# Optimization experiments

Hardware: AMD Instinct MI355X
Metric: run time of the kernel (lower is better)

The kernel has to match this reference:

```python
import jax, jax.numpy as jnp
import numpy as np

N_NODES = 50000
N_EDGES = 640000  # directed; edges (2i, 2i+1) are mutual reverses
NODE_DIM = 128
EDGE_DIM = 16
UNITS = 128
EDGE_STEPS = 4
NODE_STEPS = 4


def setup_inputs() -> dict:
    key = jax.random.key(0)
    ks = jax.random.split(key, 8)
    n_pairs = N_EDGES // 2
    a = jax.random.randint(ks[0], (n_pairs,), 0, N_NODES, dtype=jnp.int32)
    b = jax.random.randint(ks[1], (n_pairs,), 0, N_NODES, dtype=jnp.int32)
    # interleave so edge 2i = a->b and edge 2i+1 = b->a (reverse pair)
    edge_src = jnp.stack([a, b], axis=1).reshape(-1)
    edge_dst = jnp.stack([b, a], axis=1).reshape(-1)
    rev_edge = (jnp.arange(N_EDGES, dtype=jnp.int32) ^ 1)
    node_feature = jax.random.normal(ks[2], (N_NODES, NODE_DIM), jnp.float32)
    edge_feature = jax.random.normal(ks[3], (N_EDGES, EDGE_DIM), jnp.float32)
    d_in = NODE_DIM + EDGE_DIM
    W_init = jax.random.normal(ks[4], (d_in, UNITS), jnp.float32) / np.sqrt(d_in)
    b_init = jnp.zeros((UNITS,), jnp.float32)
    W_upd = jax.random.normal(ks[5], (UNITS, UNITS), jnp.float32) / np.sqrt(UNITS)
    b_upd = jnp.zeros((UNITS,), jnp.float32)
    d_node_out = UNITS + NODE_DIM
    W_node = jax.random.normal(ks[6], (d_node_out, d_node_out), jnp.float32) / np.sqrt(d_node_out)
    b_node = jnp.zeros((d_node_out,), jnp.float32)
    epsilon = jnp.zeros((), jnp.float32)
    return dict(node_feature=node_feature, edge_feature=edge_feature,
                edge_src=edge_src, edge_dst=edge_dst, rev_edge=rev_edge,
                W_init=W_init, b_init=b_init, W_upd=W_upd, b_upd=b_upd,
                W_node=W_node, b_node=b_node, epsilon=epsilon)


def reference(node_feature, edge_feature, edge_src, edge_dst, rev_edge,
              W_init, b_init, W_upd, b_upd, W_node, b_node, epsilon):
    N = node_feature.shape[0]
    # initial edge projection: concat(src node feat, edge feat) -> units, relu
    h = jax.nn.relu(
        jnp.concatenate([node_feature[edge_src], edge_feature], axis=-1) @ W_init + b_init
    )  # [E, units]
    # directed edge message passing (D-MPNN style)
    for _ in range(EDGE_STEPS):
        agg = jax.ops.segment_sum(h, edge_dst, num_segments=N)        # [N, units]
        message = agg[edge_src] - h[rev_edge]                          # exclude reverse edge
        h = jax.nn.relu(message @ W_upd + b_upd + h)
    # aggregate edges to nodes, concat with original node features
    msg = jax.ops.segment_sum(h, edge_dst, num_segments=N)             # [N, units]
    x = jnp.concatenate([node_feature, msg], axis=-1)                  # [N, units+node_dim]
    x0 = (x * (1.0 + epsilon)) @ W_node + b_node                       # GIN-style initial
    # node message passing: sum-aggregate neighbors + residual initial
    for _ in range(NODE_STEPS):
        x = jax.ops.segment_sum(x[edge_src], edge_dst, num_segments=N) + x0
    return x
```

## Files before the change

### kernel.cpp

```cpp
#include <hip/hip_runtime.h>
#include <stdint.h>

#define N_NODES 50000
#define N_EDGES 640000
#define NODE_DIM 128
#define EDGE_DIM 16
#define UNITS 128
#define DOUT 256
#define SCAN_NB ((N_NODES + 255) / 256)

typedef __attribute__((ext_vector_type(4))) float v4f;
typedef __attribute__((ext_vector_type(8))) short v8s;
typedef __attribute__((ext_vector_type(4))) short v4s;
typedef __attribute__((ext_vector_type(2))) unsigned v2u;
typedef __attribute__((ext_vector_type(4))) unsigned v4u;

static __device__ __forceinline__ short f2bf(float f) {
    return (short)((__float_as_uint(f) + 0x8000u) >> 16);
}
static __device__ __forceinline__ float bf2f(short s) {
    return __uint_as_float(((unsigned)(unsigned short)s) << 16);
}
static __device__ __forceinline__ unsigned pack_bf2(float a, float b) {
    unsigned ua = __float_as_uint(a) + 0x8000u;
    unsigned ub = __float_as_uint(b) + 0x8000u;
    return __builtin_amdgcn_perm(ub, ua, 0x07060302);
}

__global__ void k_zero(int* __restrict__ p, int n) {
    int i = blockIdx.x * 256 + threadIdx.x;
    if (i < n) p[i] = 0;
}

__global__ void k_hist(const int* __restrict__ dst, int* __restrict__ counts) {
    int e = blockIdx.x * 256 + threadIdx.x;
    if (e < N_EDGES) atomicAdd(&counts[dst[e]], 1);
}

__global__ __launch_bounds__(256) void k_scan_part(const int* __restrict__ counts,
                                                   int* __restrict__ part) {
    __shared__ int red[256];
    int t = threadIdx.x;
    int i = blockIdx.x * 256 + t;
    red[t] = (i < N_NODES) ? counts[i] : 0;
    __syncthreads();
#pragma unroll
    for (int s = 128; s > 0; s >>= 1) {
        if (t < s) red[t] += red[t + s];
        __syncthreads();
    }
    if (t == 0) part[blockIdx.x] = red[0];
}

__global__ __launch_bounds__(256) void k_scan_base(const int* __restrict__ part,
                                                   int* __restrict__ base) {
    __shared__ int buf[2][256];
    int t = threadIdx.x;
    int v = (t < SCAN_NB) ? part[t] : 0;
    buf[0][t] = v;
    __syncthreads();
    int cur = 0;
#pragma unroll
    for (int s = 1; s < 256; s <<= 1) {
        int nv = buf[cur][t];
        if (t >= s) nv += buf[cur][t - s];
        buf[cur ^ 1][t] = nv;
        cur ^= 1;
        __syncthreads();
    }
    if (t < SCAN_NB) base[t] = buf[cur][t] - v;
}

__global__ __launch_bounds__(256) void k_scan_write(const int* __restrict__ counts,
                                                    const int* __restrict__ base,
                                                    int* __restrict__ rowptr,
                                                    int* __restrict__ cursor) {
    __shared__ int buf[2][256];
    int t = threadIdx.x;
    int i = blockIdx.x * 256 + t;
    int v = (i < N_NODES) ? counts[i] : 0;
    buf[0][t] = v;
    __syncthreads();
    int cur = 0;
#pragma unroll
    for (int s = 1; s < 256; s <<= 1) {
        int nv = buf[cur][t];
        if (t >= s) nv += buf[cur][t - s];
        buf[cur ^ 1][t] = nv;
        cur ^= 1;
        __syncthreads();
    }
    if (i < N_NODES) {
        int excl = buf[cur][t] - v + base[blockIdx.x];
        rowptr[i] = excl;
        cursor[i] = excl;
    }
    if (i == 0) rowptr[N_NODES] = N_EDGES;
}

__global__ void k_fill(const int* __restrict__ src, const int* __restrict__ dst,
                       int* __restrict__ cursor, int* __restrict__ csr_eid,
                       int* __restrict__ csr_src) {
    int e = blockIdx.x * 256 + threadIdx.x;
    if (e < N_EDGES) {
        int d = dst[e];
        int pos = atomicAdd(&cursor[d], 1);
        csr_eid[pos] = e;
        csr_src[pos] = src[e];
    }
}

__global__ void k_prep(const float* __restrict__ Wi, const float* __restrict__ Wu,
                       const float* __restrict__ Wn, short* __restrict__ WtI1,
                       short* __restrict__ WtI2, short* __restrict__ WtU,
                       short* __restrict__ WtN) {
    int i = blockIdx.x * 256 + threadIdx.x;
    if (i < 128 * 128) {
        int n = i >> 7, k = i & 127;
        WtI1[i] = f2bf(Wi[k * UNITS + n]);
        return;
    }
    int j = i - 128 * 128;
    if (j < 128 * 32) {
        int n = j >> 5, k = j & 31;
        WtI2[j] = (k < EDGE_DIM) ? f2bf(Wi[(NODE_DIM + k) * UNITS + n]) : (short)0;
        return;
    }
    int l = j - 128 * 32;
    if (l < 128 * 128) {
        int n = l >> 7, k = l & 127;
        WtU[l] = f2bf(Wu[k * UNITS + n]);
        return;
    }
    int m = l - 128 * 128;
    if (m < 256 * 256) {
        int n = m >> 8, k = m & 255;
        WtN[m] = f2bf(Wn[k * DOUT + n]);
    }
}

__global__ __launch_bounds__(256) void k_nfw(
    const float* __restrict__ nf, const short* __restrict__ WtI1,
    short* __restrict__ nfw) {
    __shared__ __align__(16) short nT[32][UNITS + 8];
    int t = threadIdx.x;
    int i0 = blockIdx.x * 32;
#pragma unroll
    for (int i = 0; i < 4; ++i) {
        int idx = i * 256 + t;
        int row = idx >> 5, c4 = idx & 31;
        int ri = i0 + row; if (ri >= N_NODES) ri = N_NODES - 1;
        v4f v = *(const v4f*)&nf[(size_t)ri * NODE_DIM + c4 * 4];
        unsigned* dst = (unsigned*)&nT[row][c4 * 4];
        dst[0] = pack_bf2(v[0], v[1]);
        dst[1] = pack_bf2(v[2], v[3]);
    }
    __syncthreads();
    int w = t >> 6, lane = t & 63, quad = lane >> 4, l16 = lane & 15;
    v4f acc[2][2];
#pragma unroll
    for (int m = 0; m < 2; ++m)
#pragma unroll
        for (int n = 0; n < 2; ++n) { acc[m][n][0] = 0; acc[m][n][1] = 0; acc[m][n][2] = 0; acc[m][n][3] = 0; }
#pragma unroll
    for (int kc = 0; kc < 4; ++kc) {
        int ko = kc * 32 + quad * 8;
        v8s a0 = *(const v8s*)&nT[l16][ko];
        v8s a1 = *(const v8s*)&nT[16 + l16][ko];
        v8s b0 = *(const v8s*)&WtI1[(size_t)(w * 32 + l16) * UNITS + ko];
        v8s b1 = *(const v8s*)&WtI1[(size_t)(w * 32 + 16 + l16) * UNITS + ko];
        acc[0][0] = __builtin_amdgcn_mfma_f32_16x16x32_bf16(a0, b0, acc[0][0], 0, 0, 0);
        acc[1][0] = __builtin_amdgcn_mfma_f32_16x16x32_bf16(a1, b0, acc[1][0], 0, 0, 0);
        acc[0][1] = __builtin_amdgcn_mfma_f32_16x16x32_bf16(a0, b1, acc[0][1], 0, 0, 0);
        acc[1][1] = __builtin_amdgcn_mfma_f32_16x16x32_bf16(a1, b1, acc[1][1], 0, 0, 0);
    }
    __syncthreads();
#pragma unroll
    for (int m = 0; m < 2; ++m)
#pragma unroll
        for (int n = 0; n < 2; ++n)
#pragma unroll
            for (int r = 0; r < 4; ++r) {
                int row = m * 16 + quad * 4 + r;
                int col = w * 32 + n * 16 + l16;
                nT[row][col] = f2bf(acc[m][n][r]);
            }
    __syncthreads();
#pragma unroll
    for (int i = 0; i < 2; ++i) {
        int idx = i * 256 + t;
        int row = idx >> 4, c = idx & 15;
        if (i0 + row < N_NODES)
            *((v8s*)&nfw[(size_t)(i0 + row) * UNITS + c * 8]) = *(const v8s*)&nT[row][c * 8];
    }
}

__global__ __launch_bounds__(256) void k_edge_init2(
    const float* __restrict__ ef, const int* __restrict__ esrc,
    const short* __restrict__ nfw, const short* __restrict__ WtI2,
    const float* __restrict__ bi, short* __restrict__ h) {
    __shared__ __align__(16) short efT[64][40];
    __shared__ __align__(16) short nfwT[64][UNITS + 8];
    int t = threadIdx.x;
    int e0 = blockIdx.x * 64;
    int r0 = t >> 4, c = t & 15;
    int s0 = esrc[e0 + r0];
    int s1 = esrc[e0 + 16 + r0];
    int s2 = esrc[e0 + 32 + r0];
    int s3 = esrc[e0 + 48 + r0];
    v8s n0 = *(const v8s*)&nfw[(size_t)s0 * UNITS + c * 8];
    v8s n1 = *(const v8s*)&nfw[(size_t)s1 * UNITS + c * 8];
    v8s n2 = *(const v8s*)&nfw[(size_t)s2 * UNITS + c * 8];
    v8s n3 = *(const v8s*)&nfw[(size_t)s3 * UNITS + c * 8];
    {
        int row = t >> 2, c4 = t & 3;
        v4f v = *(const v4f*)&ef[(size_t)(e0 + row) * EDGE_DIM + c4 * 4];
        unsigned* dst = (unsigned*)&efT[row][c4 * 4];
        dst[0] = pack_bf2(v[0], v[1]);
        dst[1] = pack_bf2(v[2], v[3]);
        unsigned* z = (unsigned*)&efT[row][16 + c4 * 4];
        z[0] = 0; z[1] = 0;
    }
    *((v8s*)&nfwT[r0][c * 8]) = n0;
    *((v8s*)&nfwT[16 + r0][c * 8]) = n1;
    *((v8s*)&nfwT[32 + r0][c * 8]) = n2;
    *((v8s*)&nfwT[48 + r0][c * 8]) = n3;
    __syncthreads();
    int w = t >> 6, lane = t & 63, quad = lane >> 4, l16 = lane & 15;
    v4f acc[4][2];
#pragma unroll
    for (int m = 0; m < 4; ++m)
#pragma unroll
        for (int n = 0; n < 2; ++n) { acc[m][n][0] = 0; acc[m][n][1] = 0; acc[m][n][2] = 0; acc[m][n][3] = 0; }
    {
        int ko = quad * 8;
        v8s b0 = *(const v8s*)&WtI2[(size_t)(w * 32 + l16) * 32 + ko];
        v8s b1 = *(const v8s*)&WtI2[(size_t)(w * 32 + 16 + l16) * 32 + ko];
#pragma unroll
        for (int m = 0; m < 4; ++m) {
            v8s a = *(const v8s*)&efT[m * 16 + l16][ko];
            acc[m][0] = __builtin_amdgcn_mfma_f32_16x16x32_bf16(a, b0, acc[m][0], 0, 0, 0);
            acc[m][1] = __builtin_amdgcn_mfma_f32_16x16x32_bf16(a, b1, acc[m][1], 0, 0, 0);
        }
    }
#pragma unroll
    for (int m = 0; m < 4; ++m)
#pragma unroll
        for (int n = 0; n < 2; ++n)
#pragma unroll
            for (int r = 0; r < 4; ++r) {
                int row = m * 16 + quad * 4 + r;
                int col = w * 32 + n * 16 + l16;
                float v = acc[m][n][r] + bf2f(nfwT[row][col]) + bi[col];
                nfwT[row][col] = f2bf(fmaxf(v, 0.f));
            }
    __syncthreads();
#pragma unroll
    for (int i = 0; i < 4; ++i) {
        int idx = i * 256 + t;
        int row = idx >> 4, cc = idx & 15;
        *((v8s*)&h[(size_t)(e0 + row) * UNITS + cc * 8]) = *(const v8s*)&nfwT[row][cc * 8];
    }
}

__global__ __launch_bounds__(256) void k_agg_bf(
    const short* __restrict__ h, const int* __restrict__ rowptr,
    const int* __restrict__ csr_eid, short* __restrict__ aggb) {
    int w = threadIdx.x >> 6, lane = threadIdx.x & 63;
    int node = blockIdx.x * 4 + w;
    int g = lane >> 4, l = lane & 15;
    int beg = rowptr[node], end = rowptr[node + 1];
    int deg = end - beg;
    int ev = (lane < deg) ? csr_eid[beg + lane] : 0;
    int dcap = deg < 64 ? deg : 64;
    float a[8];
#pragma unroll
    for (int k = 0; k < 8; ++k) a[k] = 0.f;
    for (int base = 0; base < dcap; base += 8) {
        int j0 = base + g, j1 = j0 + 4;
        int ea = __shfl(ev, j0);
        int eb = __shfl(ev, j1);
        if (j1 < dcap) {
            v8s u = *(const v8s*)&h[(size_t)ea * UNITS + l * 8];
            v8s v = *(const v8s*)&h[(size_t)eb * UNITS + l * 8];
#pragma unroll
            for (int k = 0; k < 8; ++k) a[k] += bf2f(u[k]) + bf2f(v[k]);
        } else if (j0 < dcap) {
            v8s u = *(const v8s*)&h[(size_t)ea * UNITS + l * 8];
#pragma unroll
            for (int k = 0; k < 8; ++k) a[k] += bf2f(u[k]);
        }
    }
    for (int jj = 64 + g; jj < deg; jj += 4) {
        int ea = csr_eid[beg + jj];
        v8s u = *(const v8s*)&h[(size_t)ea * UNITS + l * 8];
#pragma unroll
        for (int k = 0; k < 8; ++k) a[k] += bf2f(u[k]);
    }
#pragma unroll
    for (int k = 0; k < 8; ++k) {
        a[k] += __shfl_xor(a[k], 16);
        a[k] += __shfl_xor(a[k], 32);
    }
    if (g == 0) {
        v4u o;
        o[0] = pack_bf2(a[0], a[1]); o[1] = pack_bf2(a[2], a[3]);
        o[2] = pack_bf2(a[4], a[5]); o[3] = pack_bf2(a[6], a[7]);
        *((v4u*)&aggb[(size_t)node * UNITS + l * 8]) = o;
    }
}

__global__ __launch_bounds__(256) void k_agg(
    const short* __restrict__ h, const int* __restrict__ rowptr,
    const int* __restrict__ csr_eid, float* __restrict__ agg) {
    int w = threadIdx.x >> 6, lane = threadIdx.x & 63;
    int node = blockIdx.x * 4 + w;
    int g = lane >> 4, l = lane & 15;
    int beg = rowptr[node], end = rowptr[node + 1];
    int deg = end - beg;
    int ev = (lane < deg) ? csr_eid[beg + lane] : 0;
    int dcap = deg < 64 ? deg : 64;
    float a[8];
#pragma unroll
    for (int k = 0; k < 8; ++k) a[k] = 0.f;
    for (int base = 0; base < dcap; base += 8) {
        int j0 = base + g, j1 = j0 + 4;
        int ea = __shfl(ev, j0);
        int eb = __shfl(ev, j1);
        if (j1 < dcap) {
            v8s u = *(const v8s*)&h[(size_t)ea * UNITS + l * 8];
            v8s v = *(const v8s*)&h[(size_t)eb * UNITS + l * 8];
#pragma unroll
            for (int k = 0; k < 8; ++k) a[k] += bf2f(u[k]) + bf2f(v[k]);
        } else if (j0 < dcap) {
            v8s u = *(const v8s*)&h[(size_t)ea * UNITS + l * 8];
#pragma unroll
            for (int k = 0; k < 8; ++k) a[k] += bf2f(u[k]);
        }
    }
    for (int jj = 64 + g; jj < deg; jj += 4) {
        int ea = csr_eid[beg + jj];
        v8s u = *(const v8s*)&h[(size_t)ea * UNITS + l * 8];
#pragma unroll
        for (int k = 0; k < 8; ++k) a[k] += bf2f(u[k]);
    }
#pragma unroll
    for (int k = 0; k < 8; ++k) {
        a[k] += __shfl_xor(a[k], 16);
        a[k] += __shfl_xor(a[k], 32);
    }
    if (g == 0) {
        v4f o0, o1;
        o0[0] = a[0]; o0[1] = a[1]; o0[2] = a[2]; o0[3] = a[3];
        o1[0] = a[4]; o1[1] = a[5]; o1[2] = a[6]; o1[3] = a[7];
        *((v4f*)&agg[(size_t)node * UNITS + l * 8]) = o0;
        *((v4f*)&agg[(size_t)node * UNITS + l * 8 + 4]) = o1;
    }
}

__global__ __launch_bounds__(256, 4) void k_edge_step(
    const short* __restrict__ aggb, const int* __restrict__ esrc,
    const short* __restrict__ WtU, const float* __restrict__ bu,
    short* __restrict__ h) {
    __shared__ __align__(16) short msgT[64][UNITS + 8];
    int t = threadIdx.x;
    int e0 = blockIdx.x * 64;
    int srcv[4];
#pragma unroll
    for (int i = 0; i < 4; ++i) srcv[i] = esrc[e0 + ((i * 256 + t) >> 4)];
    v8s hreg[4], areg[4];
#pragma unroll
    for (int i = 0; i < 4; ++i) {
        int idx = i * 256 + t;
        int row = idx >> 4, c = idx & 15;
        hreg[i] = *(const v8s*)&h[(size_t)(e0 + row) * UNITS + c * 8];
        areg[i] = *(const v8s*)&aggb[(size_t)srcv[i] * UNITS + c * 8];
    }
#pragma unroll
    for (int i = 0; i < 4; ++i) {
        int idx = i * 256 + t;
        int row = idx >> 4, c = idx & 15;
        v4u hv = __builtin_bit_cast(v4u, hreg[i]);
        v4u rv;
#pragma unroll
        for (int k = 0; k < 4; ++k) rv[k] = (unsigned)__shfl_xor((int)hv[k], 16);
        v8s hr = __builtin_bit_cast(v8s, rv);
        unsigned* mrow = (unsigned*)&msgT[row][c * 8];
#pragma unroll
        for (int k = 0; k < 4; ++k) {
            float d0 = bf2f(areg[i][2 * k]) - bf2f(hr[2 * k]);
            float d1 = bf2f(areg[i][2 * k + 1]) - bf2f(hr[2 * k + 1]);
            mrow[k] = pack_bf2(d0, d1);
        }
    }
    __syncthreads();
    int w = t >> 6, lane = t & 63, quad = lane >> 4, l16 = lane & 15;
    v4f acc[4][2];
#pragma unroll
    for (int m = 0; m < 4; ++m)
#pragma unroll
        for (int n = 0; n < 2; ++n) { acc[m][n][0] = 0; acc[m][n][1] = 0; acc[m][n][2] = 0; acc[m][n][3] = 0; }
#pragma unroll
    for (int kc = 0; kc < 4; ++kc) {
        int ko = kc * 32 + quad * 8;
        v8s b0 = *(const v8s*)&WtU[(size_t)(w * 32 + l16) * UNITS + ko];
        v8s b1 = *(const v8s*)&WtU[(size_t)(w * 32 + 16 + l16) * UNITS + ko];
#pragma unroll
        for (int m = 0; m < 4; ++m) {
            v8s a = *(const v8s*)&msgT[m * 16 + l16][ko];
            acc[m][0] = __builtin_amdgcn_mfma_f32_16x16x32_bf16(a, b0, acc[m][0], 0, 0, 0);
            acc[m][1] = __builtin_amdgcn_mfma_f32_16x16x32_bf16(a, b1, acc[m][1], 0, 0, 0);
        }
    }
    __syncthreads();
#pragma unroll
    for (int m = 0; m < 4; ++m)
#pragma unroll
        for (int n = 0; n < 2; ++n)
#pragma unroll
            for (int r = 0; r < 4; ++r) {
                int row = m * 16 + quad * 4 + r;
                int col = w * 32 + n * 16 + l16;
                msgT[row][col] = f2bf(acc[m][n][r] + bu[col]);
            }
    __syncthreads();
#pragma unroll
    for (int i = 0; i < 4; ++i) {
        int idx = i * 256 + t;
        int row = idx >> 4, c = idx & 15;
        v8s mv = *(const v8s*)&msgT[row][c * 8];
        v4u o;
#pragma unroll
        for (int k = 0; k < 4; ++k) {
            float v0 = fmaxf(bf2f(mv[2 * k]) + bf2f(hreg[i][2 * k]), 0.f);
            float v1 = fmaxf(bf2f(mv[2 * k + 1]) + bf2f(hreg[i][2 * k + 1]), 0.f);
            o[k] = pack_bf2(v0, v1);
        }
        *((v4u*)&h[(size_t)(e0 + row) * UNITS + c * 8]) = o;
    }
}

__global__ __launch_bounds__(256) void k_node_init(
    const float* __restrict__ nf, const float* __restrict__ msg,
    const short* __restrict__ WtN, const float* __restrict__ bn,
    const float* __restrict__ epsv, float* __restrict__ x0,
    short* __restrict__ xcatb) {
    __shared__ __align__(16) short xin[32][DOUT + 8];
    int t = threadIdx.x;
    int i0 = blockIdx.x * 32;
#pragma unroll
    for (int i = 0; i < 8; ++i) {
        int idx = i * 256 + t;
        int row = idx >> 6, c4 = idx & 63;
        int ri = i0 + row; if (ri >= N_NODES) ri = N_NODES - 1;
        int col = c4 * 4;
        v4f v;
        if (col < NODE_DIM) v = *(const v4f*)&nf[(size_t)ri * NODE_DIM + col];
        else v = *(const v4f*)&msg[(size_t)ri * UNITS + (col - NODE_DIM)];
        unsigned* dst = (unsigned*)&xin[row][col];
        dst[0] = pack_bf2(v[0], v[1]);
        dst[1] = pack_bf2(v[2], v[3]);
    }
    __syncthreads();
#pragma unroll
    for (int i = 0; i < 4; ++i) {
        int idx = i * 256 + t;
        int row = idx >> 5, c = idx & 31;
        int ri = i0 + row;
        if (ri < N_NODES) {
            v8s v = *(const v8s*)&xin[row][c * 8];
            *((v8s*)&xcatb[(size_t)ri * DOUT + c * 8]) = v;
        }
    }
    int w = t >> 6, lane = t & 63, quad = lane >> 4, l16 = lane & 15;
    v4f acc[2][4];
#pragma unroll
    for (int m = 0; m < 2; ++m)
#pragma unroll
        for (int n = 0; n < 4; ++n) { acc[m][n][0] = 0; acc[m][n][1] = 0; acc[m][n][2] = 0; acc[m][n][3] = 0; }
#pragma unroll
    for (int kc = 0; kc < 8; ++kc) {
        int ko = kc * 32 + quad * 8;
        v8s a0 = *(const v8s*)&xin[l16][ko];
        v8s a1 = *(const v8s*)&xin[16 + l16][ko];
#pragma unroll
        for (int n = 0; n < 4; ++n) {
            v8s b = *(const v8s*)&WtN[(size_t)(w * 64 + n * 16 + l16) * DOUT + ko];
            acc[0][n] = __builtin_amdgcn_mfma_f32_16x16x32_bf16(a0, b, acc[0][n], 0, 0, 0);
            acc[1][n] = __builtin_amdgcn_mfma_f32_16x16x32_bf16(a1, b, acc[1][n], 0, 0, 0);
        }
    }
    float scale = 1.f + epsv[0];
#pragma unroll
    for (int m = 0; m < 2; ++m)
#pragma unroll
        for (int n = 0; n < 4; ++n)
#pragma unroll
            for (int r = 0; r < 4; ++r) {
                int row = m * 16 + quad * 4 + r;
                int col = w * 64 + n * 16 + l16;
                if (i0 + row < N_NODES)
                    x0[(size_t)(i0 + row) * DOUT + col] = acc[m][n][r] * scale + bn[col];
            }
}

__global__ __launch_bounds__(256) void k_node_step_b(
    const short* __restrict__ xb, const float* __restrict__ x0,
    const int* __restrict__ rowptr, const int* __restrict__ csr_src,
    short* __restrict__ outb, float* __restrict__ outf, int writef) {
    int w = threadIdx.x >> 6, lane = threadIdx.x & 63;
    int node = blockIdx.x * 4 + w;
    int beg = rowptr[node], end = rowptr[node + 1];
    int deg = end - beg;
    int sv = (lane < deg) ? csr_src[beg + lane] : 0;
    int dcap = deg < 64 ? deg : 64;
    v4f xv = *(const v4f*)&x0[(size_t)node * DOUT + lane * 4];
    float a0 = xv[0], a1 = xv[1], a2 = xv[2], a3 = xv[3];
    float b0 = 0, b1 = 0, b2 = 0, b3 = 0;
    int j = 0;
    for (; j + 4 <= dcap; j += 4) {
        int s0 = __shfl(sv, j), s1 = __shfl(sv, j + 1);
        int s2 = __shfl(sv, j + 2), s3 = __shfl(sv, j + 3);
        v4s u0 = *(const v4s*)&xb[(size_t)s0 * DOUT + lane * 4];
        v4s u1 = *(const v4s*)&xb[(size_t)s1 * DOUT + lane * 4];
        v4s u2 = *(const v4s*)&xb[(size_t)s2 * DOUT + lane * 4];
        v4s u3 = *(const v4s*)&xb[(size_t)s3 * DOUT + lane * 4];
        a0 += bf2f(u0[0]) + bf2f(u1[0]); b0 += bf2f(u2[0]) + bf2f(u3[0]);
        a1 += bf2f(u0[1]) + bf2f(u1[1]); b1 += bf2f(u2[1]) + bf2f(u3[1]);
        a2 += bf2f(u0[2]) + bf2f(u1[2]); b2 += bf2f(u2[2]) + bf2f(u3[2]);
        a3 += bf2f(u0[3]) + bf2f(u1[3]); b3 += bf2f(u2[3]) + bf2f(u3[3]);
    }
    for (; j < dcap; ++j) {
        int s0 = __shfl(sv, j);
        v4s u0 = *(const v4s*)&xb[(size_t)s0 * DOUT + lane * 4];
        a0 += bf2f(u0[0]); a1 += bf2f(u0[1]); a2 += bf2f(u0[2]); a3 += bf2f(u0[3]);
    }
    for (int jj = 64; jj < deg; ++jj) {
        int s0 = csr_src[beg + jj];
        v4s u0 = *(const v4s*)&xb[(size_t)s0 * DOUT + lane * 4];
        a0 += bf2f(u0[0]); a1 += bf2f(u0[1]); a2 += bf2f(u0[2]); a3 += bf2f(u0[3]);
    }
    a0 += b0; a1 += b1; a2 += b2; a3 += b3;
    if (writef) {
        v4f o; o[0] = a0; o[1] = a1; o[2] = a2; o[3] = a3;
        *((v4f*)&outf[(size_t)node * DOUT + lane * 4]) = o;
    } else {
        v2u o; o[0] = pack_bf2(a0, a1); o[1] = pack_bf2(a2, a3);
        *((v2u*)&outb[(size_t)node * DOUT + lane * 4]) = o;
    }
}

extern "C" void kernel_launch(void* const* d_in, const int* in_sizes, int n_in,
                              void* d_out, int out_size, void* d_ws, size_t ws_size,
                              hipStream_t stream) {
    const float* nf  = (const float*)d_in[0];
    const float* ef  = (const float*)d_in[1];
    const int* esrc  = (const int*)d_in[2];
    const int* edst  = (const int*)d_in[3];
    const float* Wi  = (const float*)d_in[5];
    const float* bi  = (const float*)d_in[6];
    const float* Wu  = (const float*)d_in[7];
    const float* bu  = (const float*)d_in[8];
    const float* Wn  = (const float*)d_in[9];
    const float* bn  = (const float*)d_in[10];
    const float* eps = (const float*)d_in[11];

    char* ws = (char*)d_ws;
    size_t off = 0;
    auto alloc = [&](size_t bytes) -> char* {
        char* p = ws + off;
        off += (bytes + 255) & ~(size_t)255;
        return p;
    };
    short* h     = (short*)alloc((size_t)N_EDGES * UNITS * 2);
    float* x0    = (float*)h;
    short* xcatb = (short*)((char*)h + (size_t)N_NODES * DOUT * 4);
    short* xbA   = (short*)((char*)xcatb + (size_t)N_NODES * DOUT * 2);
    short* xbB   = (short*)((char*)xbA + (size_t)N_NODES * DOUT * 2);
    char*  R     = alloc((size_t)N_NODES * UNITS * 4);
    short* nfw   = (short*)R;
    short* aggb  = (short*)(R + (size_t)N_NODES * UNITS * 2);
    float* agg   = (float*)R;
    int* counts  = (int*)alloc((size_t)N_NODES * 4);
    int* rowptr  = (int*)alloc((size_t)(N_NODES + 1) * 4);
    int* cursor  = (int*)alloc((size_t)N_NODES * 4);
    int* part    = (int*)alloc((size_t)SCAN_NB * 4);
    int* base    = (int*)alloc((size_t)SCAN_NB * 4);
    int* csr_eid = (int*)alloc((size_t)N_EDGES * 4);
    int* csr_src = (int*)alloc((size_t)N_EDGES * 4);
    short* WtI1  = (short*)alloc((size_t)128 * 128 * 2);
    short* WtI2  = (short*)alloc((size_t)128 * 32 * 2);
    short* WtU   = (short*)alloc((size_t)128 * 128 * 2);
    short* WtN   = (short*)alloc((size_t)256 * 256 * 2);
    float* xout  = (float*)d_out;

    if (ws_size < off) return;

    k_zero<<<(N_NODES + 255) / 256, 256, 0, stream>>>(counts, N_NODES);
    k_hist<<<(N_EDGES + 255) / 256, 256, 0, stream>>>(edst, counts);
    k_scan_part<<<SCAN_NB, 256, 0, stream>>>(counts, part);
    k_scan_base<<<1, 256, 0, stream>>>(part, base);
    k_scan_write<<<SCAN_NB, 256, 0, stream>>>(counts, base, rowptr, cursor);
    k_fill<<<(N_EDGES + 255) / 256, 256, 0, stream>>>(esrc, edst, cursor, csr_eid, csr_src);
    k_prep<<<(128 * 128 + 128 * 32 + 128 * 128 + 256 * 256 + 255) / 256, 256, 0, stream>>>(
        Wi, Wu, Wn, WtI1, WtI2, WtU, WtN);

    k_nfw<<<(N_NODES + 31) / 32, 256, 0, stream>>>(nf, WtI1, nfw);
    k_edge_init2<<<N_EDGES / 64, 256, 0, stream>>>(ef, esrc, nfw, WtI2, bi, h);
    for (int s = 0; s < 4; ++s) {
        k_agg_bf<<<N_NODES / 4, 256, 0, stream>>>(h, rowptr, csr_eid, aggb);
        k_edge_step<<<N_EDGES / 64, 256, 0, stream>>>(aggb, esrc, WtU, bu, h);
    }
    k_agg<<<N_NODES / 4, 256, 0, stream>>>(h, rowptr, csr_eid, agg);
    k_node_init<<<(N_NODES + 31) / 32, 256, 0, stream>>>(nf, agg, WtN, bn, eps, x0, xcatb);
    k_node_step_b<<<N_NODES / 4, 256, 0, stream>>>(xcatb, x0, rowptr, csr_src, xbA, nullptr, 0);
    k_node_step_b<<<N_NODES / 4, 256, 0, stream>>>(xbA, x0, rowptr, csr_src, xbB, nullptr, 0);
    k_node_step_b<<<N_NODES / 4, 256, 0, stream>>>(xbB, x0, rowptr, csr_src, xbA, nullptr, 0);
    k_node_step_b<<<N_NODES / 4, 256, 0, stream>>>(xbA, x0, rowptr, csr_src, nullptr, xout, 1);
}
```

Measured before the change: 960.8 us.

## Batch gather loads in aggregation kernels and double-tile edge step

The aggregation kernels now issue four or eight independent gather loads per iteration and mask out-of-range entries with a multiply-by-zero FMA instead of branching, which raises memory-level parallelism. The edge-step kernel handles two 64-edge tiles per block and prefetches the second tile's h and aggregate rows into registers while the first tile's MFMA runs. To leave room for the extra registers, the occupancy hint drops from 4 to 3 blocks per SM. The masked loads read from whatever edge index the shuffle returns for invalid slots, so some loads are wasted. The costs are that extra traffic and the lower occupancy.

```diff
diff --git a/kernel.cpp b/kernel.cpp
--- a/kernel.cpp
+++ b/kernel.cpp
@@ -276,20 +276,21 @@
     float a[8];
 #pragma unroll
     for (int k = 0; k < 8; ++k) a[k] = 0.f;
-    for (int base = 0; base < dcap; base += 8) {
-        int j0 = base + g, j1 = j0 + 4;
-        int ea = __shfl(ev, j0);
-        int eb = __shfl(ev, j1);
-        if (j1 < dcap) {
-            v8s u = *(const v8s*)&h[(size_t)ea * UNITS + l * 8];
-            v8s v = *(const v8s*)&h[(size_t)eb * UNITS + l * 8];
-#pragma unroll
-            for (int k = 0; k < 8; ++k) a[k] += bf2f(u[k]) + bf2f(v[k]);
-        } else if (j0 < dcap) {
-            v8s u = *(const v8s*)&h[(size_t)ea * UNITS + l * 8];
-#pragma unroll
-            for (int k = 0; k < 8; ++k) a[k] += bf2f(u[k]);
-        }
+    for (int base = 0; base < dcap; base += 16) {
+        v8s u[4];
+        float m[4];
+#pragma unroll
+        for (int q = 0; q < 4; ++q) {
+            int jq = base + g + 4 * q;
+            int eq = __shfl(ev, jq);
+            u[q] = *(const v8s*)&h[(size_t)eq * UNITS + l * 8];
+            m[q] = (jq < dcap) ? 1.f : 0.f;
+        }
+#pragma unroll
+        for (int q = 0; q < 4; ++q)
+#pragma unroll
+            for (int k = 0; k < 8; ++k)
+                a[k] = fmaf(m[q], bf2f(u[q][k]), a[k]);
     }
     for (int jj = 64 + g; jj < deg; jj += 4) {
         int ea = csr_eid[beg + jj];
@@ -323,20 +324,21 @@
     float a[8];
 #pragma unroll
     for (int k = 0; k < 8; ++k) a[k] = 0.f;
-    for (int base = 0; base < dcap; base += 8) {
-        int j0 = base + g, j1 = j0 + 4;
-        int ea = __shfl(ev, j0);
-        int eb = __shfl(ev, j1);
-        if (j1 < dcap) {
-            v8s u = *(const v8s*)&h[(size_t)ea * UNITS + l * 8];
-            v8s v = *(const v8s*)&h[(size_t)eb * UNITS + l * 8];
-#pragma unroll
-            for (int k = 0; k < 8; ++k) a[k] += bf2f(u[k]) + bf2f(v[k]);
-        } else if (j0 < dcap) {
-            v8s u = *(const v8s*)&h[(size_t)ea * UNITS + l * 8];
-#pragma unroll
-            for (int k = 0; k < 8; ++k) a[k] += bf2f(u[k]);
-        }
+    for (int base = 0; base < dcap; base += 16) {
+        v8s u[4];
+        float m[4];
+#pragma unroll
+        for (int q = 0; q < 4; ++q) {
+            int jq = base + g + 4 * q;
+            int eq = __shfl(ev, jq);
+            u[q] = *(const v8s*)&h[(size_t)eq * UNITS + l * 8];
+            m[q] = (jq < dcap) ? 1.f : 0.f;
+        }
+#pragma unroll
+        for (int q = 0; q < 4; ++q)
+#pragma unroll
+            for (int k = 0; k < 8; ++k)
+                a[k] = fmaf(m[q], bf2f(u[q][k]), a[k]);
     }
     for (int jj = 64 + g; jj < deg; jj += 4) {
         int ea = csr_eid[beg + jj];
@@ -358,29 +360,30 @@
     }
 }
 
-__global__ __launch_bounds__(256, 4) void k_edge_step(
+__global__ __launch_bounds__(256, 3) void k_edge_step(
     const short* __restrict__ aggb, const int* __restrict__ esrc,
     const short* __restrict__ WtU, const float* __restrict__ bu,
     short* __restrict__ h) {
     __shared__ __align__(16) short msgT[64][UNITS + 8];
     int t = threadIdx.x;
-    int e0 = blockIdx.x * 64;
-    int srcv[4];
-#pragma unroll
-    for (int i = 0; i < 4; ++i) srcv[i] = esrc[e0 + ((i * 256 + t) >> 4)];
-    v8s hreg[4], areg[4];
+    int eA = blockIdx.x * 128;
+    int eB = eA + 64;
+    int w = t >> 6, lane = t & 63, quad = lane >> 4, l16 = lane & 15;
+
+    v8s hA[4], aA[4];
 #pragma unroll
     for (int i = 0; i < 4; ++i) {
         int idx = i * 256 + t;
         int row = idx >> 4, c = idx & 15;
-        hreg[i] = *(const v8s*)&h[(size_t)(e0 + row) * UNITS + c * 8];
-        areg[i] = *(const v8s*)&aggb[(size_t)srcv[i] * UNITS + c * 8];
+        int s = esrc[eA + row];
+        hA[i] = *(const v8s*)&h[(size_t)(eA + row) * UNITS + c * 8];
+        aA[i] = *(const v8s*)&aggb[(size_t)s * UNITS + c * 8];
     }
 #pragma unroll
     for (int i = 0; i < 4; ++i) {
         int idx = i * 256 + t;
         int row = idx >> 4, c = idx & 15;
-        v4u hv = __builtin_bit_cast(v4u, hreg[i]);
+        v4u hv = __builtin_bit_cast(v4u, hA[i]);
         v4u rv;
 #pragma unroll
         for (int k = 0; k < 4; ++k) rv[k] = (unsigned)__shfl_xor((int)hv[k], 16);
@@ -388,41 +391,51 @@
         unsigned* mrow = (unsigned*)&msgT[row][c * 8];
 #pragma unroll
         for (int k = 0; k < 4; ++k) {
-            float d0 = bf2f(areg[i][2 * k]) - bf2f(hr[2 * k]);
-            float d1 = bf2f(areg[i][2 * k + 1]) - bf2f(hr[2 * k + 1]);
+            float d0 = bf2f(aA[i][2 * k]) - bf2f(hr[2 * k]);
+            float d1 = bf2f(aA[i][2 * k + 1]) - bf2f(hr[2 * k + 1]);
             mrow[k] = pack_bf2(d0, d1);
         }
     }
     __syncthreads();
-    int w = t >> 6, lane = t & 63, quad = lane >> 4, l16 = lane & 15;
-    v4f acc[4][2];
-#pragma unroll
-    for (int m = 0; m < 4; ++m)
-#pragma unroll
-        for (int n = 0; n < 2; ++n) { acc[m][n][0] = 0; acc[m][n][1] = 0; acc[m][n][2] = 0; acc[m][n][3] = 0; }
-#pragma unroll
-    for (int kc = 0; kc < 4; ++kc) {
-        int ko = kc * 32 + quad * 8;
-        v8s b0 = *(const v8s*)&WtU[(size_t)(w * 32 + l16) * UNITS + ko];
-        v8s b1 = *(const v8s*)&WtU[(size_t)(w * 32 + 16 + l16) * UNITS + ko];
-#pragma unroll
-        for (int m = 0; m < 4; ++m) {
-            v8s a = *(const v8s*)&msgT[m * 16 + l16][ko];
-            acc[m][0] = __builtin_amdgcn_mfma_f32_16x16x32_bf16(a, b0, acc[m][0], 0, 0, 0);
-            acc[m][1] = __builtin_amdgcn_mfma_f32_16x16x32_bf16(a, b1, acc[m][1], 0, 0, 0);
-        }
-    }
-    __syncthreads();
-#pragma unroll
-    for (int m = 0; m < 4; ++m)
-#pragma unroll
-        for (int n = 0; n < 2; ++n)
-#pragma unroll
-            for (int r = 0; r < 4; ++r) {
-                int row = m * 16 + quad * 4 + r;
-                int col = w * 32 + n * 16 + l16;
-                msgT[row][col] = f2bf(acc[m][n][r] + bu[col]);
+    v8s hB[4], aB[4];
+#pragma unroll
+    for (int i = 0; i < 4; ++i) {
+        int idx = i * 256 + t;
+        int row = idx >> 4, c = idx & 15;
+        int s = esrc[eB + row];
+        hB[i] = *(const v8s*)&h[(size_t)(eB + row) * UNITS + c * 8];
+        aB[i] = *(const v8s*)&aggb[(size_t)s * UNITS + c * 8];
+    }
+    {
+        v4f acc[4][2];
+#pragma unroll
+        for (int m = 0; m < 4; ++m)
+#pragma unroll
+            for (int n = 0; n < 2; ++n) { acc[m][n][0] = 0; acc[m][n][1] = 0; acc[m][n][2] = 0; acc[m][n][3] = 0; }
+#pragma unroll
+        for (int kc = 0; kc < 4; ++kc) {
+            int ko = kc * 32 + quad * 8;
+            v8s b0 = *(const v8s*)&WtU[(size_t)(w * 32 + l16) * UNITS + ko];
+            v8s b1 = *(const v8s*)&WtU[(size_t)(w * 32 + 16 + l16) * UNITS + ko];
+#pragma unroll
+            for (int m = 0; m < 4; ++m) {
+                v8s a = *(const v8s*)&msgT[m * 16 + l16][ko];
+                acc[m][0] = __builtin_amdgcn_mfma_f32_16x16x32_bf16(a, b0, acc[m][0], 0, 0, 0);
+                acc[m][1] = __builtin_amdgcn_mfma_f32_16x16x32_bf16(a, b1, acc[m][1], 0, 0, 0);
             }
+        }
+        __syncthreads();
+#pragma unroll
+        for (int m = 0; m < 4; ++m)
+#pragma unroll
+            for (int n = 0; n < 2; ++n)
+#pragma unroll
+                for (int r = 0; r < 4; ++r) {
+                    int row = m * 16 + quad * 4 + r;
+                    int col = w * 32 + n * 16 + l16;
+                    msgT[row][col] = f2bf(acc[m][n][r] + bu[col]);
+                }
+    }
     __syncthreads();
 #pragma unroll
     for (int i = 0; i < 4; ++i) {
@@ -432,11 +445,75 @@
         v4u o;
 #pragma unroll
         for (int k = 0; k < 4; ++k) {
-            float v0 = fmaxf(bf2f(mv[2 * k]) + bf2f(hreg[i][2 * k]), 0.f);
-            float v1 = fmaxf(bf2f(mv[2 * k + 1]) + bf2f(hreg[i][2 * k + 1]), 0.f);
+            float v0 = fmaxf(bf2f(mv[2 * k]) + bf2f(hA[i][2 * k]), 0.f);
+            float v1 = fmaxf(bf2f(mv[2 * k + 1]) + bf2f(hA[i][2 * k + 1]), 0.f);
             o[k] = pack_bf2(v0, v1);
         }
-        *((v4u*)&h[(size_t)(e0 + row) * UNITS + c * 8]) = o;
+        *((v4u*)&h[(size_t)(eA + row) * UNITS + c * 8]) = o;
+    }
+    __syncthreads();
+#pragma unroll
+    for (int i = 0; i < 4; ++i) {
+        int idx = i * 256 + t;
+        int row = idx >> 4, c = idx & 15;
+        v4u hv = __builtin_bit_cast(v4u, hB[i]);
+        v4u rv;
+#pragma unroll
+        for (int k = 0; k < 4; ++k) rv[k] = (unsigned)__shfl_xor((int)hv[k], 16);
+        v8s hr = __builtin_bit_cast(v8s, rv);
+        unsigned* mrow = (unsigned*)&msgT[row][c * 8];
+#pragma unroll
+        for (int k = 0; k < 4; ++k) {
+            float d0 = bf2f(aB[i][2 * k]) - bf2f(hr[2 * k]);
+            float d1 = bf2f(aB[i][2 * k + 1]) - bf2f(hr[2 * k + 1]);
+            mrow[k] = pack_bf2(d0, d1);
+        }
+    }
+    __syncthreads();
+    {
+        v4f acc[4][2];
+#pragma unroll
+        for (int m = 0; m < 4; ++m)
+#pragma unroll
+            for (int n = 0; n < 2; ++n) { acc[m][n][0] = 0; acc[m][n][1] = 0; acc[m][n][2] = 0; acc[m][n][3] = 0; }
+#pragma unroll
+        for (int kc = 0; kc < 4; ++kc) {
+            int ko = kc * 32 + quad * 8;
+            v8s b0 = *(const v8s*)&WtU[(size_t)(w * 32 + l16) * UNITS + ko];
+            v8s b1 = *(const v8s*)&WtU[(size_t)(w * 32 + 16 + l16) * UNITS + ko];
+#pragma unroll
+            for (int m = 0; m < 4; ++m) {
+                v8s a = *(const v8s*)&msgT[m * 16 + l16][ko];
+                acc[m][0] = __builtin_amdgcn_mfma_f32_16x16x32_bf16(a, b0, acc[m][0], 0, 0, 0);
+                acc[m][1] = __builtin_amdgcn_mfma_f32_16x16x32_bf16(a, b1, acc[m][1], 0, 0, 0);
+            }
+        }
+        __syncthreads();
+#pragma unroll
+        for (int m = 0; m < 4; ++m)
+#pragma unroll
+            for (int n = 0; n < 2; ++n)
+#pragma unroll
+                for (int r = 0; r < 4; ++r) {
+                    int row = m * 16 + quad * 4 + r;
+                    int col = w * 32 + n * 16 + l16;
+                    msgT[row][col] = f2bf(acc[m][n][r] + bu[col]);
+                }
+    }
+    __syncthreads();
+#pragma unroll
+    for (int i = 0; i < 4; ++i) {
+        int idx = i * 256 + t;
+        int row = idx >> 4, c = idx & 15;
+        v8s mv = *(const v8s*)&msgT[row][c * 8];
+        v4u o;
+#pragma unroll
+        for (int k = 0; k < 4; ++k) {
+            float v0 = fmaxf(bf2f(mv[2 * k]) + bf2f(hB[i][2 * k]), 0.f);
+            float v1 = fmaxf(bf2f(mv[2 * k + 1]) + bf2f(hB[i][2 * k + 1]), 0.f);
+            o[k] = pack_bf2(v0, v1);
+        }
+        *((v4u*)&h[(size_t)(eB + row) * UNITS + c * 8]) = o;
     }
 }
 
@@ -516,31 +593,29 @@
     int dcap = deg < 64 ? deg : 64;
     v4f xv = *(const v4f*)&x0[(size_t)node * DOUT + lane * 4];
     float a0 = xv[0], a1 = xv[1], a2 = xv[2], a3 = xv[3];
-    float b0 = 0, b1 = 0, b2 = 0, b3 = 0;
-    int j = 0;
-    for (; j + 4 <= dcap; j += 4) {
-        int s0 = __shfl(sv, j), s1 = __shfl(sv, j + 1);
-        int s2 = __shfl(sv, j + 2), s3 = __shfl(sv, j + 3);
-        v4s u0 = *(const v4s*)&xb[(size_t)s0 * DOUT + lane * 4];
-        v4s u1 = *(const v4s*)&xb[(size_t)s1 * DOUT + lane * 4];
-        v4s u2 = *(const v4s*)&xb[(size_t)s2 * DOUT + lane * 4];
-        v4s u3 = *(const v4s*)&xb[(size_t)s3 * DOUT + lane * 4];
-        a0 += bf2f(u0[0]) + bf2f(u1[0]); b0 += bf2f(u2[0]) + bf2f(u3[0]);
-        a1 += bf2f(u0[1]) + bf2f(u1[1]); b1 += bf2f(u2[1]) + bf2f(u3[1]);
-        a2 += bf2f(u0[2]) + bf2f(u1[2]); b2 += bf2f(u2[2]) + bf2f(u3[2]);
-        a3 += bf2f(u0[3]) + bf2f(u1[3]); b3 += bf2f(u2[3]) + bf2f(u3[3]);
-    }
-    for (; j < dcap; ++j) {
-        int s0 = __shfl(sv, j);
-        v4s u0 = *(const v4s*)&xb[(size_t)s0 * DOUT + lane * 4];
-        a0 += bf2f(u0[0]); a1 += bf2f(u0[1]); a2 += bf2f(u0[2]); a3 += bf2f(u0[3]);
+    for (int base = 0; base < dcap; base += 8) {
+        v4s u[8];
+        float m[8];
+#pragma unroll
+        for (int q = 0; q < 8; ++q) {
+            int jq = base + q;
+            int sq = __shfl(sv, jq);
+            u[q] = *(const v4s*)&xb[(size_t)sq * DOUT + lane * 4];
+            m[q] = (jq < dcap) ? 1.f : 0.f;
+        }
+#pragma unroll
+        for (int q = 0; q < 8; ++q) {
+            a0 = fmaf(m[q], bf2f(u[q][0]), a0);
+            a1 = fmaf(m[q], bf2f(u[q][1]), a1);
+            a2 = fmaf(m[q], bf2f(u[q][2]), a2);
+            a3 = fmaf(m[q], bf2f(u[q][3]), a3);
+        }
     }
     for (int jj = 64; jj < deg; ++jj) {
         int s0 = csr_src[beg + jj];
         v4s u0 = *(const v4s*)&xb[(size_t)s0 * DOUT + lane * 4];
         a0 += bf2f(u0[0]); a1 += bf2f(u0[1]); a2 += bf2f(u0[2]); a3 += bf2f(u0[3]);
     }
-    a0 += b0; a1 += b1; a2 += b2; a3 += b3;
     if (writef) {
         v4f o; o[0] = a0; o[1] = a1; o[2] = a2; o[3] = a3;
         *((v4f*)&outf[(size_t)node * DOUT + lane * 4]) = o;
@@ -609,7 +684,7 @@
     k_edge_init2<<<N_EDGES / 64, 256, 0, stream>>>(ef, esrc, nfw, WtI2, bi, h);
     for (int s = 0; s < 4; ++s) {
         k_agg_bf<<<N_NODES / 4, 256, 0, stream>>>(h, rowptr, csr_eid, aggb);
-        k_edge_step<<<N_EDGES / 64, 256, 0, stream>>>(aggb, esrc, WtU, bu, h);
+        k_edge_step<<<N_EDGES / 128, 256, 0, stream>>>(aggb, esrc, WtU, bu, h);
     }
     k_agg<<<N_NODES / 4, 256, 0, stream>>>(h, rowptr, csr_eid, agg);
     k_node_init<<<(N_NODES + 31) / 32, 256, 0, stream>>>(nf, agg, WtN, bn, eps, x0, xcatb);
```

After: 987.3 us. 1.03x slower.
